# Kernel tuning notes

Hardware: AMD Instinct MI355X
Metric: run time of the kernel (lower is better)

Reference implementation:

```python
import jax, jax.numpy as jnp
import numpy as np

B, D = 8192, 768
TOP_K = 5


def setup_inputs() -> dict:
    key = jax.random.key(0)
    ks = jax.random.split(key, 12)
    # xavier_uniform bound for (D, D)
    bg = float(np.sqrt(6.0 / (D + D)))
    def xav(k, fan_in, fan_out):
        b = float(np.sqrt(6.0 / (fan_in + fan_out)))
        return jax.random.uniform(k, (fan_in, fan_out), jnp.float32, -b, b)
    return {
        "X": jax.random.normal(ks[0], (B, D), jnp.float32),
        "A_ecfp": jax.random.uniform(ks[1], (B, B), jnp.float32),
        "W_g": jax.random.uniform(ks[2], (D, D), jnp.float32, -bg, bg),
        "raw_alpha": jnp.zeros((), jnp.float32),
        "W_gcn": xav(ks[3], D, D),
        "b_gcn": jnp.zeros((D,), jnp.float32),
        "W1": xav(ks[4], D, 512),
        "b1": jnp.zeros((512,), jnp.float32),
        "W2": xav(ks[5], 512, 256),
        "b2": jnp.zeros((256,), jnp.float32),
        "W3": xav(ks[6], 256, 1),
        "b3": jnp.zeros((1,), jnp.float32),
    }


def _forward(X, A_ecfp, W_g, raw_alpha, W_gcn, b_gcn, W1, b1, W2, b2, W3, b3):
    n = X.shape[0]
    # learned similarity, blended with ECFP prior
    S = jax.nn.relu((X @ W_g) @ X.T)                    # (B, B)
    alpha = jax.nn.sigmoid(raw_alpha)
    A = alpha * A_ecfp + (1.0 - alpha) * S
    # top-k sparsification per row, symmetrized (OR)
    k = min(TOP_K, n - 1)
    _, top_idx = jax.lax.top_k(A, k)                    # (B, k)
    rows = jnp.arange(n)[:, None]
    mask = jnp.zeros_like(A).at[rows, top_idx].set(1.0)
    mask = ((mask + mask.T) > 0).astype(A.dtype)
    A = A * mask
    # zero diagonal, then add self-loops (diagonal becomes 1)
    diag = jnp.eye(n, dtype=A.dtype)
    A = A * (1.0 - diag) + diag
    # degree normalization D^-1 A
    D_inv = 1.0 / jnp.clip(A.sum(-1, keepdims=True), 1e-8)
    A_norm = A * D_inv
    # single GCN layer (exact erf GELU, matching torch default)
    H = jax.nn.gelu(A_norm @ X @ W_gcn + b_gcn, approximate=False)
    # MLP head (dropout is identity in eval)
    h = jax.nn.gelu(H @ W1 + b1, approximate=False)
    h = jax.nn.gelu(h @ W2 + b2, approximate=False)
    return h @ W3 + b3                                  # (B, 1)


def reference(X, A_ecfp, W_g, raw_alpha, W_gcn, b_gcn, W1, b1, W2, b2, W3, b3):
    return _forward(X, A_ecfp, W_g, raw_alpha, W_gcn, b_gcn, W1, b1, W2, b2, W3, b3)
```

## Files before the change

### kernel.cpp

```cpp
#include <hip/hip_runtime.h>
#include <math.h>


typedef __attribute__((ext_vector_type(8))) short short8v;
typedef __attribute__((ext_vector_type(4))) float f32x4;

__device__ __forceinline__ unsigned short f2bf(float f) {
  unsigned u = __float_as_uint(f);
  u += 0x7fffu + ((u >> 16) & 1u);
  return (unsigned short)(u >> 16);
}
__device__ __forceinline__ float bf2f(unsigned short h) {
  return __uint_as_float(((unsigned)h) << 16);
}
__device__ __forceinline__ float gelu_f(float x) {
  return 0.5f * x * (1.f + erff(x * 0.7071067811865475f));
}
__device__ __forceinline__ void gload16(const void* g, void* l) {
  __builtin_amdgcn_global_load_lds(
      (const __attribute__((address_space(1))) unsigned int*)g,
      (__attribute__((address_space(3))) unsigned int*)l, 16, 0, 0);
}

template <int N>
__device__ __forceinline__ void insN(float v, int j, float (&lv)[N], int (&li)[N]) {
#pragma unroll
  for (int p = N - 1; p >= 1; --p) {
    bool shiftv = v > lv[p - 1];
    bool here = (v > lv[p]) && !shiftv;
    float nv = shiftv ? lv[p - 1] : (here ? v : lv[p]);
    int ni = shiftv ? li[p - 1] : (here ? j : li[p]);
    lv[p] = nv; li[p] = ni;
  }
  if (v > lv[0]) { lv[0] = v; li[0] = j; }
}

__global__ __launch_bounds__(256) void cvt_bf16(const float* __restrict__ in,
                                                unsigned short* __restrict__ out, int n4) {
  int t = blockIdx.x * 256 + threadIdx.x;
  if (t >= n4) return;
  float4 f = ((const float4*)in)[t];
  ushort4 r;
  r.x = f2bf(f.x); r.y = f2bf(f.y); r.z = f2bf(f.z); r.w = f2bf(f.w);
  ((ushort4*)out)[t] = r;
}

__global__ __launch_bounds__(256) void split2(const float* __restrict__ in,
                                              unsigned short* __restrict__ out,
                                              int K, int n4) {
  int t = blockIdx.x * 256 + threadIdx.x;
  if (t >= n4) return;
  int kq = K >> 2;
  int row = t / kq, c4 = t - row * kq;
  float4 f = ((const float4*)in)[t];
  ushort4 h, l;
  float x;
  x = f.x; h.x = f2bf(x); l.x = f2bf(x - bf2f(h.x));
  x = f.y; h.y = f2bf(x); l.y = f2bf(x - bf2f(h.y));
  x = f.z; h.z = f2bf(x); l.z = f2bf(x - bf2f(h.z));
  x = f.w; h.w = f2bf(x); l.w = f2bf(x - bf2f(h.w));
  *(ushort4*)(out + (size_t)row * 2 * K + c4 * 4) = h;
  *(ushort4*)(out + (size_t)row * 2 * K + K + c4 * 4) = l;
}

__global__ __launch_bounds__(256) void split_wt2(const float* __restrict__ W,
                                                 unsigned short* __restrict__ t2,
                                                 int K, int N) {
  __shared__ float tile[32][33];
  int kb = blockIdx.x * 32, nb = blockIdx.y * 32;
  int tx = threadIdx.x & 31, ty = threadIdx.x >> 5;
#pragma unroll
  for (int p = 0; p < 4; ++p)
    tile[ty + p * 8][tx] = W[(size_t)(kb + ty + p * 8) * N + nb + tx];
  __syncthreads();
#pragma unroll
  for (int p = 0; p < 4; ++p) {
    int n = ty + p * 8;
    float x = tile[tx][n];
    unsigned short h = f2bf(x);
    unsigned short l = f2bf(x - bf2f(h));
    t2[(size_t)(nb + n) * (2 * K) + kb + tx] = h;
    t2[(size_t)(nb + n) * (2 * K) + K + kb + tx] = l;
  }
}

__global__ __launch_bounds__(256) void sgemm_f32(const float* __restrict__ A,
                                                 const float* __restrict__ Bm,
                                                 float* __restrict__ C,
                                                 unsigned short* __restrict__ Cbf,
                                                 int N, int K) {
  __shared__ float As[2][16][68];
  __shared__ float Bs[2][16][132];
  const int r0 = blockIdx.x * 64, c0 = blockIdx.y * 128;
  const int tid = threadIdx.x;
  const int tr = tid >> 4, tc = tid & 15;
  const int lrow = tid >> 2, lkq = tid & 3;
  const int kk0 = tid >> 5, nq = tid & 31;
  float acc[4][8];
#pragma unroll
  for (int i = 0; i < 4; ++i)
#pragma unroll
    for (int j = 0; j < 8; ++j) acc[i][j] = 0.f;

  const int nk = K >> 4;
  float4 aR = *(const float4*)(A + (size_t)(r0 + lrow) * K + lkq * 4);
  float4 bR0 = *(const float4*)(Bm + (size_t)kk0 * N + c0 + nq * 4);
  float4 bR1 = *(const float4*)(Bm + (size_t)(kk0 + 8) * N + c0 + nq * 4);
  As[0][lkq * 4 + 0][lrow] = aR.x; As[0][lkq * 4 + 1][lrow] = aR.y;
  As[0][lkq * 4 + 2][lrow] = aR.z; As[0][lkq * 4 + 3][lrow] = aR.w;
  *(float4*)&Bs[0][kk0][nq * 4] = bR0;
  *(float4*)&Bs[0][kk0 + 8][nq * 4] = bR1;
  __syncthreads();

  int cur = 0;
  for (int t = 0; t < nk; ++t) {
    if (t < nk - 1) {
      int kn = (t + 1) * 16;
      aR = *(const float4*)(A + (size_t)(r0 + lrow) * K + kn + lkq * 4);
      bR0 = *(const float4*)(Bm + (size_t)(kn + kk0) * N + c0 + nq * 4);
      bR1 = *(const float4*)(Bm + (size_t)(kn + kk0 + 8) * N + c0 + nq * 4);
    }
#pragma unroll
    for (int k = 0; k < 16; ++k) {
      float a[4], b[8];
      *(float4*)&a[0] = *(const float4*)&As[cur][k][tr * 4];
      *(float4*)&b[0] = *(const float4*)&Bs[cur][k][tc * 8];
      *(float4*)&b[4] = *(const float4*)&Bs[cur][k][tc * 8 + 4];
#pragma unroll
      for (int i = 0; i < 4; ++i)
#pragma unroll
        for (int j = 0; j < 8; ++j) acc[i][j] = fmaf(a[i], b[j], acc[i][j]);
    }
    if (t < nk - 1) {
      int nxt = cur ^ 1;
      As[nxt][lkq * 4 + 0][lrow] = aR.x; As[nxt][lkq * 4 + 1][lrow] = aR.y;
      As[nxt][lkq * 4 + 2][lrow] = aR.z; As[nxt][lkq * 4 + 3][lrow] = aR.w;
      *(float4*)&Bs[nxt][kk0][nq * 4] = bR0;
      *(float4*)&Bs[nxt][kk0 + 8][nq * 4] = bR1;
    }
    __syncthreads();
    cur ^= 1;
  }
#pragma unroll
  for (int i = 0; i < 4; ++i) {
    int r = r0 + tr * 4 + i;
#pragma unroll
    for (int jq = 0; jq < 2; ++jq) {
      *(float4*)(C + (size_t)r * N + c0 + tc * 8 + jq * 4) = *(float4*)&acc[i][jq * 4];
      ushort4 hb;
      hb.x = f2bf(acc[i][jq * 4 + 0]); hb.y = f2bf(acc[i][jq * 4 + 1]);
      hb.z = f2bf(acc[i][jq * 4 + 2]); hb.w = f2bf(acc[i][jq * 4 + 3]);
      *(ushort4*)(Cbf + (size_t)r * N + c0 + tc * 8 + jq * 4) = hb;
    }
  }
}

template <int EPI>
__global__ __launch_bounds__(256) void gemm_bt(const unsigned short* __restrict__ A,
                                               const unsigned short* __restrict__ Bt,
                                               const float* __restrict__ bias,
                                               float* __restrict__ C,
                                               unsigned short* __restrict__ C2,
                                               int N, int K) {
  __shared__ __align__(16) unsigned short As[2 * 128 * 64];
  __shared__ __align__(16) unsigned short Bs[2 * 128 * 64];
  const int r0 = blockIdx.x * 128, c0 = blockIdx.y * 128;
  const int tid = threadIdx.x, lane = tid & 63, w = tid >> 6;
  const int wr = w >> 1, wc = w & 1;
  f32x4 acc[4][4];
  const f32x4 z4 = {0.f, 0.f, 0.f, 0.f};
#pragma unroll
  for (int i = 0; i < 4; ++i)
#pragma unroll
    for (int j = 0; j < 4; ++j) acc[i][j] = z4;

  const int srow = w * 32 + (lane >> 3);
  const int ksl = (lane & 7) ^ (lane >> 3);
  const unsigned short* aSrc = A + (size_t)(r0 + srow) * K + ksl * 8;
  const unsigned short* bSrc = Bt + (size_t)(c0 + srow) * K + ksl * 8;
  const int rsw = (lane & 7);
  const int nk = K >> 6;

#pragma unroll
  for (int t4 = 0; t4 < 4; ++t4) {
    gload16(aSrc + (size_t)t4 * 8 * K, (char*)As + (w * 32 + t4 * 8) * 128);
    gload16(bSrc + (size_t)t4 * 8 * K, (char*)Bs + (w * 32 + t4 * 8) * 128);
  }
  __syncthreads();

  int cur = 0;
  for (int kt = 0; kt < nk; ++kt) {
    if (kt < nk - 1) {
      const int kn = (kt + 1) * 64;
      const int off = (cur ^ 1) * 16384;
#pragma unroll
      for (int t4 = 0; t4 < 4; ++t4) {
        gload16(aSrc + kn + (size_t)t4 * 8 * K, (char*)As + off + (w * 32 + t4 * 8) * 128);
        gload16(bSrc + kn + (size_t)t4 * 8 * K, (char*)Bs + off + (w * 32 + t4 * 8) * 128);
      }
    }
    const int cbase = cur * 16384;
#pragma unroll
    for (int ks = 0; ks < 2; ++ks) {
      short8v af[4], bf[4];
      const int slot = (((ks * 4 + (lane >> 4)) ^ rsw) << 4) + cbase;
#pragma unroll
      for (int f = 0; f < 4; ++f) {
        af[f] = *(const short8v*)((const char*)As + (wr * 64 + f * 16 + (lane & 15)) * 128 + slot);
        bf[f] = *(const short8v*)((const char*)Bs + (wc * 64 + f * 16 + (lane & 15)) * 128 + slot);
      }
#pragma unroll
      for (int fi = 0; fi < 4; ++fi)
#pragma unroll
        for (int fj = 0; fj < 4; ++fj)
          acc[fi][fj] = __builtin_amdgcn_mfma_f32_16x16x32_bf16(af[fi], bf[fj], acc[fi][fj], 0, 0, 0);
    }
    __syncthreads();
    cur ^= 1;
  }
#pragma unroll
  for (int fi = 0; fi < 4; ++fi)
#pragma unroll
    for (int fj = 0; fj < 4; ++fj) {
      int col = c0 + wc * 64 + fj * 16 + (lane & 15);
      int rowb = r0 + wr * 64 + fi * 16 + (lane >> 4) * 4;
#pragma unroll
      for (int r = 0; r < 4; ++r) {
        float x = acc[fi][fj][r];
        if constexpr (EPI == 0) {
          C[(size_t)(rowb + r) * N + col] = x;
        } else if constexpr (EPI == 1) {
          C[(size_t)(rowb + r) * N + col] = gelu_f(x + bias[col]);
        } else {
          float y = gelu_f(x + bias[col]);
          unsigned short h = f2bf(y);
          unsigned short l = f2bf(y - bf2f(h));
          C2[(size_t)(rowb + r) * 2 * N + col] = h;
          C2[(size_t)(rowb + r) * 2 * N + N + col] = l;
        }
      }
    }
}

__global__ __launch_bounds__(512, 4) void s_topk(const unsigned short* __restrict__ Gh,
                                                 const unsigned short* __restrict__ Xh,
                                                 float* __restrict__ pv, int* __restrict__ pix) {
  __shared__ __align__(16) unsigned short As[2 * 128 * 64];
  __shared__ __align__(16) unsigned short Bs[2 * 128 * 64];
  const int bid = blockIdx.x;
  const int p = bid & 7, q = bid >> 3;
  const int r0 = (p * 8 + (q & 7)) * 128;
  const int chunk = q >> 3;
  const int tid = threadIdx.x, lane = tid & 63, w = tid >> 6;
  const int wr = w >> 2, wc = w & 3;
  float lv0[5], lv1[5]; int li0[5], li1[5];
#pragma unroll
  for (int q2 = 0; q2 < 5; ++q2) {
    lv0[q2] = -1e30f; li0[q2] = 0; lv1[q2] = -1e30f; li1[q2] = 0;
  }

  const int strow = tid >> 3, sslot = tid & 7;
  const int ksl = sslot ^ (strow & 7);
  const unsigned short* bSrc = Gh + (size_t)(r0 + strow) * 768 + ksl * 8;
  char* aDst0 = (char*)As + strow * 128 + sslot * 16;
  char* bDst0 = (char*)Bs + strow * 128 + sslot * 16;
  const int rsw = lane & 7;

  {
    const unsigned short* a0 = Xh + (size_t)(chunk * 1024 + strow) * 768 + ksl * 8;
    gload16(a0, aDst0);
    gload16(a0 + (size_t)64 * 768, aDst0 + 8192);
    gload16(bSrc, bDst0);
    gload16(bSrc + (size_t)64 * 768, bDst0 + 8192);
  }
  __syncthreads();

  int cur = 0;
  for (int jt = 0; jt < 8; ++jt) {
    const int j0 = chunk * 1024 + jt * 128;
    const unsigned short* aSrc = Xh + (size_t)(j0 + strow) * 768 + ksl * 8;
    f32x4 acc[4][2];
    const f32x4 z4 = {0.f, 0.f, 0.f, 0.f};
#pragma unroll
    for (int i = 0; i < 4; ++i) {
      acc[i][0] = z4; acc[i][1] = z4;
    }

    for (int t = 0; t < 12; ++t) {
      const int off = (cur ^ 1) * 16384;
      if (t < 11) {
        const int kn = (t + 1) * 64;
        gload16(aSrc + kn, aDst0 + off);
        gload16(aSrc + kn + (size_t)64 * 768, aDst0 + off + 8192);
        gload16(bSrc + kn, bDst0 + off);
        gload16(bSrc + kn + (size_t)64 * 768, bDst0 + off + 8192);
      } else if (jt < 7) {
        const unsigned short* aN = aSrc + (size_t)128 * 768;
        gload16(aN, aDst0 + off);
        gload16(aN + (size_t)64 * 768, aDst0 + off + 8192);
        gload16(bSrc, bDst0 + off);
        gload16(bSrc + (size_t)64 * 768, bDst0 + off + 8192);
      }
      const int cbase = cur * 16384;
#pragma unroll
      for (int ks = 0; ks < 2; ++ks) {
        short8v aj[4], bi[2];
        const int slot = (((ks * 4 + (lane >> 4)) ^ rsw) << 4) + cbase;
#pragma unroll
        for (int f = 0; f < 4; ++f)
          aj[f] = *(const short8v*)((const char*)As + (wr * 64 + f * 16 + (lane & 15)) * 128 + slot);
#pragma unroll
        for (int f = 0; f < 2; ++f)
          bi[f] = *(const short8v*)((const char*)Bs + (wc * 32 + f * 16 + (lane & 15)) * 128 + slot);
#pragma unroll
        for (int fi = 0; fi < 4; ++fi) {
          acc[fi][0] = __builtin_amdgcn_mfma_f32_16x16x32_bf16(aj[fi], bi[0], acc[fi][0], 0, 0, 0);
          acc[fi][1] = __builtin_amdgcn_mfma_f32_16x16x32_bf16(aj[fi], bi[1], acc[fi][1], 0, 0, 0);
        }
      }
      __syncthreads();
      cur ^= 1;
    }
    const int jb = j0 + wr * 64 + (lane >> 4) * 4;
#pragma unroll
    for (int fi = 0; fi < 4; ++fi)
#pragma unroll
      for (int r = 0; r < 4; ++r) {
        int jj = jb + fi * 16 + r;
        float v0 = acc[fi][0][r];
        if (v0 > lv0[4]) insN<5>(v0, jj, lv0, li0);
        float v1 = acc[fi][1][r];
        if (v1 > lv1[4]) insN<5>(v1, jj, lv1, li1);
      }
  }
  const int slotw = wr * 4 + (lane >> 4);
  const int ib0 = r0 + wc * 32 + (lane & 15);
  size_t base0 = (((size_t)ib0 * 8 + chunk) * 8 + slotw) * 5;
#pragma unroll
  for (int q2 = 0; q2 < 5; ++q2) { pv[base0 + q2] = lv0[q2]; pix[base0 + q2] = li0[q2]; }
  size_t base1 = (((size_t)(ib0 + 16) * 8 + chunk) * 8 + slotw) * 5;
#pragma unroll
  for (int q2 = 0; q2 < 5; ++q2) { pv[base1 + q2] = lv1[q2]; pix[base1 + q2] = li1[q2]; }
}

__global__ __launch_bounds__(256) void merge16(const float* __restrict__ pv,
                                               const int* __restrict__ pix,
                                               int* __restrict__ gidx) {
  int row = blockIdx.x * 256 + threadIdx.x;
  float lv[16]; int li[16];
#pragma unroll
  for (int q = 0; q < 16; ++q) { lv[q] = -1e30f; li[q] = 0; }
  for (int ch = 0; ch < 8; ++ch)
#pragma unroll
    for (int sl = 0; sl < 8; ++sl) {
      size_t base = (((size_t)row * 8 + ch) * 8 + sl) * 5;
#pragma unroll
      for (int q = 0; q < 5; ++q) {
        float v = pv[base + q];
        if (v > lv[15]) insN<16>(v, pix[base + q], lv, li);
      }
    }
#pragma unroll
  for (int q = 0; q < 16; ++q) gidx[row * 16 + q] = li[q];
}

__global__ __launch_bounds__(256) void refine5(const float* __restrict__ G,
                                               const float* __restrict__ X,
                                               const float* __restrict__ Ae,
                                               const int* __restrict__ gidx,
                                               const float* __restrict__ ralpha,
                                               int* __restrict__ t5i, float* __restrict__ t5v) {
  int i = blockIdx.x * 4 + (threadIdx.x >> 6);
  int lane = threadIdx.x & 63;
  int c = lane >> 2, s = lane & 3;
  float sa = 1.f / (1.f + expf(-ralpha[0]));
  int j = gidx[i * 16 + c];
  const float* g = G + (size_t)i * 768;
  const float* x = X + (size_t)j * 768;
  float a = 0.f;
#pragma unroll 8
  for (int t = 0; t < 192; ++t) a = fmaf(g[s + 4 * t], x[s + 4 * t], a);
  a += __shfl_xor(a, 1);
  a += __shfl_xor(a, 2);
  float v = sa * Ae[(size_t)i * 8192 + j] + (1.f - sa) * fmaxf(a, 0.f);
  float vs[16]; int js[16];
#pragma unroll
  for (int q = 0; q < 16; ++q) { vs[q] = __shfl(v, q * 4); js[q] = __shfl(j, q * 4); }
  if (lane == 0) {
    unsigned used = 0;
#pragma unroll
    for (int t = 0; t < 5; ++t) {
      float bv = -1e30f; int bj = 0; int bq = 0; bool any = false;
#pragma unroll
      for (int q = 0; q < 16; ++q) {
        bool ok = ((used >> q) & 1u) == 0u;
        bool better = ok && (!any || vs[q] > bv || (vs[q] == bv && js[q] < bj));
        bv = better ? vs[q] : bv; bj = better ? js[q] : bj; bq = better ? q : bq;
        any = any || better;
      }
      used |= (1u << bq);
      t5v[(size_t)i * 5 + t] = bv;
      t5i[(size_t)i * 5 + t] = bj;
    }
  }
}

__global__ void edge_deg(const int* __restrict__ t5i, int* __restrict__ deg) {
  int e = blockIdx.x * 256 + threadIdx.x;
  if (e >= 40960) return;
  int i = e / 5, t = e - i * 5;
  int j = t5i[i * 5 + t];
  if (j == i) return;
  bool rev = false;
#pragma unroll
  for (int u = 0; u < 5; ++u) rev = rev || (t5i[j * 5 + u] == i);
  if (!rev || i < j) { atomicAdd(&deg[i], 1); atomicAdd(&deg[j], 1); }
}

__global__ void scan8k(const int* __restrict__ deg, int* __restrict__ off) {
  __shared__ int sums[256];
  int tid = threadIdx.x;
  int base = tid * 32;
  int s = 0;
  for (int u = 0; u < 32; ++u) s += deg[base + u];
  sums[tid] = s;
  __syncthreads();
  for (int d = 1; d < 256; d <<= 1) {
    int v = (tid >= d) ? sums[tid - d] : 0;
    __syncthreads();
    sums[tid] += v;
    __syncthreads();
  }
  int run = tid ? sums[tid - 1] : 0;
  for (int u = 0; u < 32; ++u) { off[base + u] = run; run += deg[base + u]; }
  if (tid == 255) off[8192] = run;
}

__global__ __launch_bounds__(256) void edge_fill(const int* __restrict__ t5i,
                                                 const float* __restrict__ t5v,
                                                 const float* __restrict__ G,
                                                 const float* __restrict__ X,
                                                 const float* __restrict__ Ae,
                                                 const float* __restrict__ ralpha,
                                                 const int* __restrict__ off,
                                                 int* __restrict__ cursor,
                                                 int* __restrict__ ccol, float* __restrict__ cval) {
  int e = blockIdx.x * 4 + (threadIdx.x >> 6);
  if (e >= 40960) return;
  int lane = threadIdx.x & 63;
  int i = e / 5, t = e - i * 5;
  int j = t5i[i * 5 + t];
  if (j == i) return;
  int rev = -1;
#pragma unroll
  for (int u = 0; u < 5; ++u)
    if (t5i[j * 5 + u] == i) rev = u;
  if (!(rev < 0 || i < j)) return;
  float vji;
  if (rev >= 0) {
    vji = t5v[j * 5 + rev];
  } else {
    const float* g = G + (size_t)j * 768;
    const float* x = X + (size_t)i * 768;
    float a = 0.f;
#pragma unroll
    for (int u = 0; u < 12; ++u) a = fmaf(g[lane + 64 * u], x[lane + 64 * u], a);
#pragma unroll
    for (int d = 32; d; d >>= 1) a += __shfl_xor(a, d);
    float sa = 1.f / (1.f + expf(-ralpha[0]));
    vji = sa * Ae[(size_t)j * 8192 + i] + (1.f - sa) * fmaxf(a, 0.f);
  }
  if (lane == 0) {
    float vij = t5v[i * 5 + t];
    int p0 = off[i] + atomicAdd(&cursor[i], 1);
    ccol[p0] = j; cval[p0] = vij;
    int p1 = off[j] + atomicAdd(&cursor[j], 1);
    ccol[p1] = i; cval[p1] = vji;
  }
}

__global__ __launch_bounds__(256) void gather_gcn(const float* __restrict__ X,
                                                  const int* __restrict__ off,
                                                  const int* __restrict__ ccol,
                                                  const float* __restrict__ cval,
                                                  float* __restrict__ M) {
  __shared__ float red[256];
  __shared__ float sdinv;
  int i = blockIdx.x, tid = threadIdx.x;
  int s0 = off[i], cnt = off[i + 1] - s0;
  float s = 0.f;
  for (int e = tid; e < cnt; e += 256) s += cval[s0 + e];
  red[tid] = s;
  __syncthreads();
  for (int d = 128; d; d >>= 1) {
    if (tid < d) red[tid] += red[tid + d];
    __syncthreads();
  }
  if (tid == 0) sdinv = 1.f / fmaxf(1.f + red[0], 1e-8f);
  __syncthreads();
  float dinv = sdinv;
  const float* xi = X + (size_t)i * 768;
  float a0 = xi[tid], a1 = xi[tid + 256], a2 = xi[tid + 512];
  for (int e = 0; e < cnt; ++e) {
    float v = cval[s0 + e];
    const float* xr = X + (size_t)ccol[s0 + e] * 768;
    a0 = fmaf(v, xr[tid], a0);
    a1 = fmaf(v, xr[tid + 256], a1);
    a2 = fmaf(v, xr[tid + 512], a2);
  }
  float* mi = M + (size_t)i * 768;
  mi[tid] = a0 * dinv; mi[tid + 256] = a1 * dinv; mi[tid + 512] = a2 * dinv;
}

__global__ __launch_bounds__(256) void final_head(const float* __restrict__ h2,
                                                  const float* __restrict__ W3,
                                                  const float* __restrict__ b3,
                                                  float* __restrict__ out) {
  int i = blockIdx.x * 4 + (threadIdx.x >> 6);
  int lane = threadIdx.x & 63;
  const float* r = h2 + (size_t)i * 256;
  float s = r[lane] * W3[lane] + r[lane + 64] * W3[lane + 64] +
            r[lane + 128] * W3[lane + 128] + r[lane + 192] * W3[lane + 192];
#pragma unroll
  for (int d = 32; d; d >>= 1) s += __shfl_xor(s, d);
  if (lane == 0) out[i] = s + b3[0];
}

extern "C" void kernel_launch(void* const* d_in, const int* in_sizes, int n_in,
                              void* d_out, int out_size, void* d_ws, size_t ws_size,
                              hipStream_t stream) {
  const float* X   = (const float*)d_in[0];
  const float* Ae  = (const float*)d_in[1];
  const float* Wg  = (const float*)d_in[2];
  const float* ra  = (const float*)d_in[3];
  const float* Wgc = (const float*)d_in[4];
  const float* bgc = (const float*)d_in[5];
  const float* W1  = (const float*)d_in[6];
  const float* b1  = (const float*)d_in[7];
  const float* W2  = (const float*)d_in[8];
  const float* b2  = (const float*)d_in[9];
  const float* W3  = (const float*)d_in[10];
  const float* b3  = (const float*)d_in[11];
  float* out = (float*)d_out;

  char* w = (char*)d_ws;
  size_t off_ = 0;
  auto take = [&](size_t n) -> void* {
    void* p = w + off_;
    off_ += (n + 255) & ~(size_t)255;
    return p;
  };
  float* G            = (float*)take((size_t)8192 * 768 * 4);
  unsigned short* Xh  = (unsigned short*)take((size_t)8192 * 768 * 2);
  unsigned short* Gh  = (unsigned short*)take((size_t)8192 * 768 * 2);
  float* pv           = (float*)take((size_t)8192 * 320 * 4);
  int* pix            = (int*)take((size_t)8192 * 320 * 4);
  int* gidx           = (int*)take((size_t)8192 * 16 * 4);
  int* t5i            = (int*)take((size_t)8192 * 5 * 4);
  float* t5v          = (float*)take((size_t)8192 * 5 * 4);
  int* deg            = (int*)take((size_t)8192 * 4);
  int* offr           = (int*)take((size_t)8193 * 4);
  int* cur            = (int*)take((size_t)8192 * 4);
  int* ccol           = (int*)take((size_t)81920 * 4);
  float* cval         = (float*)take((size_t)81920 * 4);
  unsigned short* Wc2 = (unsigned short*)take((size_t)768 * 1536 * 2);
  unsigned short* W12 = (unsigned short*)take((size_t)512 * 1536 * 2);
  unsigned short* W22 = (unsigned short*)take((size_t)256 * 1024 * 2);

  float* Mf            = (float*)Xh;
  unsigned short* Hp2  = (unsigned short*)Xh;
  unsigned short* A2   = (unsigned short*)G;
  unsigned short* h1p2 = (unsigned short*)G;
  float* h2f = (float*)pv;

  sgemm_f32<<<dim3(128, 6), 256, 0, stream>>>(X, Wg, G, Gh, 768, 768);
  cvt_bf16<<<6144, 256, 0, stream>>>(X, Xh, 1572864);
  split_wt2<<<dim3(24, 24), 256, 0, stream>>>(Wgc, Wc2, 768, 768);
  split_wt2<<<dim3(24, 16), 256, 0, stream>>>(W1, W12, 768, 512);
  split_wt2<<<dim3(16, 8), 256, 0, stream>>>(W2, W22, 512, 256);

  s_topk<<<512, 512, 0, stream>>>(Gh, Xh, pv, pix);
  merge16<<<32, 256, 0, stream>>>(pv, pix, gidx);
  refine5<<<2048, 256, 0, stream>>>(G, X, Ae, gidx, ra, t5i, t5v);

  hipMemsetAsync(deg, 0, 8192 * 4, stream);
  hipMemsetAsync(cur, 0, 8192 * 4, stream);
  edge_deg<<<160, 256, 0, stream>>>(t5i, deg);
  scan8k<<<1, 256, 0, stream>>>(deg, offr);
  edge_fill<<<10240, 256, 0, stream>>>(t5i, t5v, G, X, Ae, ra, offr, cur, ccol, cval);

  gather_gcn<<<8192, 256, 0, stream>>>(X, offr, ccol, cval, Mf);

  split2<<<6144, 256, 0, stream>>>(Mf, A2, 768, 1572864);
  gemm_bt<2><<<dim3(64, 6), 256, 0, stream>>>(A2, Wc2, bgc, nullptr, Hp2, 768, 1536);

  gemm_bt<2><<<dim3(64, 4), 256, 0, stream>>>(Hp2, W12, b1, nullptr, h1p2, 512, 1536);

  gemm_bt<1><<<dim3(64, 2), 256, 0, stream>>>(h1p2, W22, b2, h2f, nullptr, 256, 1024);

  final_head<<<2048, 256, 0, stream>>>(h2f, W3, b3, out);

  (void)in_sizes; (void)n_in; (void)out_size; (void)ws_size;
}
```

Baseline: 661.1 us.

## Enlarge s_topk tile to 256 rows per block for more MFMA reuse

The similarity/top-k kernel now has each block cover 256 query rows instead of 128, with each wave computing a 64x64 output tile (4x4 MFMA fragments) and keeping four running top-5 lists. The aim is to raise arithmetic intensity and reuse of each loaded X tile. The grid drops from 512 to 256 blocks. The cost is more registers and LDS per block and launch bounds relaxed to one block per CU, so occupancy and latency hiding are lower.

```diff
diff --git a/kernel.cpp b/kernel.cpp
--- a/kernel.cpp
+++ b/kernel.cpp
@@ -242,105 +242,106 @@
     }
 }
 
-__global__ __launch_bounds__(512, 4) void s_topk(const unsigned short* __restrict__ Gh,
+__global__ __launch_bounds__(512, 1) void s_topk(const unsigned short* __restrict__ Gh,
                                                  const unsigned short* __restrict__ Xh,
                                                  float* __restrict__ pv, int* __restrict__ pix) {
   __shared__ __align__(16) unsigned short As[2 * 128 * 64];
-  __shared__ __align__(16) unsigned short Bs[2 * 128 * 64];
+  __shared__ __align__(16) unsigned short Bs[2 * 256 * 64];
   const int bid = blockIdx.x;
   const int p = bid & 7, q = bid >> 3;
-  const int r0 = (p * 8 + (q & 7)) * 128;
-  const int chunk = q >> 3;
+  const int r0i = (p * 4 + (q & 3)) * 256;
+  const int chunk = q >> 2;
   const int tid = threadIdx.x, lane = tid & 63, w = tid >> 6;
-  const int wr = w >> 2, wc = w & 3;
-  float lv0[5], lv1[5]; int li0[5], li1[5];
-#pragma unroll
-  for (int q2 = 0; q2 < 5; ++q2) {
-    lv0[q2] = -1e30f; li0[q2] = 0; lv1[q2] = -1e30f; li1[q2] = 0;
-  }
-
-  const int strow = tid >> 3, sslot = tid & 7;
-  const int ksl = sslot ^ (strow & 7);
-  const unsigned short* bSrc = Gh + (size_t)(r0 + strow) * 768 + ksl * 8;
-  char* aDst0 = (char*)As + strow * 128 + sslot * 16;
-  char* bDst0 = (char*)Bs + strow * 128 + sslot * 16;
+  const int jh = w >> 2, iq = w & 3;
+  float lv[4][5]; int li[4][5];
+#pragma unroll
+  for (int f = 0; f < 4; ++f)
+#pragma unroll
+    for (int q2 = 0; q2 < 5; ++q2) { lv[f][q2] = -1e30f; li[f][q2] = 0; }
+
+  const int srow8 = tid >> 3, sslot = tid & 7;
+  const int ksl = sslot ^ (srow8 & 7);
+  const unsigned short* bS = Gh + (size_t)(r0i + srow8) * 768 + ksl * 8;
+  char* aDst = (char*)As + tid * 16;
+  char* bDst = (char*)Bs + tid * 16;
   const int rsw = lane & 7;
 
   {
-    const unsigned short* a0 = Xh + (size_t)(chunk * 1024 + strow) * 768 + ksl * 8;
-    gload16(a0, aDst0);
-    gload16(a0 + (size_t)64 * 768, aDst0 + 8192);
-    gload16(bSrc, bDst0);
-    gload16(bSrc + (size_t)64 * 768, bDst0 + 8192);
+    const unsigned short* aS0 = Xh + (size_t)(chunk * 1024 + srow8) * 768 + ksl * 8;
+#pragma unroll
+    for (int c = 0; c < 2; ++c) gload16(aS0 + (size_t)(64 * c) * 768, aDst + c * 8192);
+#pragma unroll
+    for (int c = 0; c < 4; ++c) gload16(bS + (size_t)(64 * c) * 768, bDst + c * 8192);
   }
   __syncthreads();
 
   int cur = 0;
   for (int jt = 0; jt < 8; ++jt) {
     const int j0 = chunk * 1024 + jt * 128;
-    const unsigned short* aSrc = Xh + (size_t)(j0 + strow) * 768 + ksl * 8;
-    f32x4 acc[4][2];
+    const unsigned short* aS = Xh + (size_t)(j0 + srow8) * 768 + ksl * 8;
+    f32x4 acc[4][4];
     const f32x4 z4 = {0.f, 0.f, 0.f, 0.f};
 #pragma unroll
-    for (int i = 0; i < 4; ++i) {
-      acc[i][0] = z4; acc[i][1] = z4;
-    }
+    for (int i = 0; i < 4; ++i)
+#pragma unroll
+      for (int j = 0; j < 4; ++j) acc[i][j] = z4;
 
     for (int t = 0; t < 12; ++t) {
-      const int off = (cur ^ 1) * 16384;
+      const int offA = (cur ^ 1) * 16384;
+      const int offB = (cur ^ 1) * 32768;
       if (t < 11) {
         const int kn = (t + 1) * 64;
-        gload16(aSrc + kn, aDst0 + off);
-        gload16(aSrc + kn + (size_t)64 * 768, aDst0 + off + 8192);
-        gload16(bSrc + kn, bDst0 + off);
-        gload16(bSrc + kn + (size_t)64 * 768, bDst0 + off + 8192);
+#pragma unroll
+        for (int c = 0; c < 2; ++c) gload16(aS + kn + (size_t)(64 * c) * 768, aDst + offA + c * 8192);
+#pragma unroll
+        for (int c = 0; c < 4; ++c) gload16(bS + kn + (size_t)(64 * c) * 768, bDst + offB + c * 8192);
       } else if (jt < 7) {
-        const unsigned short* aN = aSrc + (size_t)128 * 768;
-        gload16(aN, aDst0 + off);
-        gload16(aN + (size_t)64 * 768, aDst0 + off + 8192);
-        gload16(bSrc, bDst0 + off);
-        gload16(bSrc + (size_t)64 * 768, bDst0 + off + 8192);
-      }
-      const int cbase = cur * 16384;
+        const unsigned short* aN = aS + (size_t)128 * 768;
+#pragma unroll
+        for (int c = 0; c < 2; ++c) gload16(aN + (size_t)(64 * c) * 768, aDst + offA + c * 8192);
+#pragma unroll
+        for (int c = 0; c < 4; ++c) gload16(bS + (size_t)(64 * c) * 768, bDst + offB + c * 8192);
+      }
+      const int cA = cur * 16384, cB = cur * 32768;
 #pragma unroll
       for (int ks = 0; ks < 2; ++ks) {
-        short8v aj[4], bi[2];
-        const int slot = (((ks * 4 + (lane >> 4)) ^ rsw) << 4) + cbase;
-#pragma unroll
-        for (int f = 0; f < 4; ++f)
-          aj[f] = *(const short8v*)((const char*)As + (wr * 64 + f * 16 + (lane & 15)) * 128 + slot);
-#pragma unroll
-        for (int f = 0; f < 2; ++f)
-          bi[f] = *(const short8v*)((const char*)Bs + (wc * 32 + f * 16 + (lane & 15)) * 128 + slot);
-#pragma unroll
-        for (int fi = 0; fi < 4; ++fi) {
-          acc[fi][0] = __builtin_amdgcn_mfma_f32_16x16x32_bf16(aj[fi], bi[0], acc[fi][0], 0, 0, 0);
-          acc[fi][1] = __builtin_amdgcn_mfma_f32_16x16x32_bf16(aj[fi], bi[1], acc[fi][1], 0, 0, 0);
+        short8v aj[4], bi[4];
+        const int slot = ((ks * 4 + (lane >> 4)) ^ rsw) << 4;
+#pragma unroll
+        for (int f = 0; f < 4; ++f) {
+          aj[f] = *(const short8v*)((const char*)As + (jh * 64 + f * 16 + (lane & 15)) * 128 + slot + cA);
+          bi[f] = *(const short8v*)((const char*)Bs + (iq * 64 + f * 16 + (lane & 15)) * 128 + slot + cB);
         }
+#pragma unroll
+        for (int fi = 0; fi < 4; ++fi)
+#pragma unroll
+          for (int fj = 0; fj < 4; ++fj)
+            acc[fi][fj] = __builtin_amdgcn_mfma_f32_16x16x32_bf16(aj[fi], bi[fj], acc[fi][fj], 0, 0, 0);
       }
       __syncthreads();
       cur ^= 1;
     }
-    const int jb = j0 + wr * 64 + (lane >> 4) * 4;
+    const int jb = j0 + jh * 64 + (lane >> 4) * 4;
 #pragma unroll
     for (int fi = 0; fi < 4; ++fi)
 #pragma unroll
       for (int r = 0; r < 4; ++r) {
-        int jj = jb + fi * 16 + r;
-        float v0 = acc[fi][0][r];
-        if (v0 > lv0[4]) insN<5>(v0, jj, lv0, li0);
-        float v1 = acc[fi][1][r];
-        if (v1 > lv1[4]) insN<5>(v1, jj, lv1, li1);
-      }
-  }
-  const int slotw = wr * 4 + (lane >> 4);
-  const int ib0 = r0 + wc * 32 + (lane & 15);
-  size_t base0 = (((size_t)ib0 * 8 + chunk) * 8 + slotw) * 5;
-#pragma unroll
-  for (int q2 = 0; q2 < 5; ++q2) { pv[base0 + q2] = lv0[q2]; pix[base0 + q2] = li0[q2]; }
-  size_t base1 = (((size_t)(ib0 + 16) * 8 + chunk) * 8 + slotw) * 5;
-#pragma unroll
-  for (int q2 = 0; q2 < 5; ++q2) { pv[base1 + q2] = lv1[q2]; pix[base1 + q2] = li1[q2]; }
+        const int jj = jb + fi * 16 + r;
+#pragma unroll
+        for (int fj = 0; fj < 4; ++fj) {
+          float v = acc[fi][fj][r];
+          if (v > lv[fj][4]) insN<5>(v, jj, lv[fj], li[fj]);
+        }
+      }
+  }
+  const int slotw = jh * 4 + (lane >> 4);
+#pragma unroll
+  for (int fj = 0; fj < 4; ++fj) {
+    const int ib = r0i + iq * 64 + fj * 16 + (lane & 15);
+    size_t base = (((size_t)ib * 8 + chunk) * 8 + slotw) * 5;
+#pragma unroll
+    for (int q2 = 0; q2 < 5; ++q2) { pv[base + q2] = lv[fj][q2]; pix[base + q2] = li[fj][q2]; }
+  }
 }
 
 __global__ __launch_bounds__(256) void merge16(const float* __restrict__ pv,
@@ -579,7 +580,7 @@
   split_wt2<<<dim3(24, 16), 256, 0, stream>>>(W1, W12, 768, 512);
   split_wt2<<<dim3(16, 8), 256, 0, stream>>>(W2, W22, 512, 256);
 
-  s_topk<<<512, 512, 0, stream>>>(Gh, Xh, pv, pix);
+  s_topk<<<256, 512, 0, stream>>>(Gh, Xh, pv, pix);
   merge16<<<32, 256, 0, stream>>>(pv, pix, gidx);
   refine5<<<2048, 256, 0, stream>>>(G, X, Ae, gidx, ra, t5i, t5v);
 
```

Result: slower. 694.0 us (+5.0%).
